# Kernel optimization log

Measured on AMD Instinct MI355X. Metric: run time of the kernel, lower is better.

The kernel has to match this reference:

```python
import jax, jax.numpy as jnp
import numpy as np

N_ITER = 2
EPS = 1e-06
EPS2 = 1e-06
EPS3 = 0.001

B, F, M, T = 8, 513, 8, 512


def setup_inputs() -> dict:
    key = jax.random.key(0)
    k1, k2, k3, k4, k5 = jax.random.split(key, 5)
    r = jax.random.uniform(k1, (B, F, M, T), dtype=jnp.float32) + 0.1  # positive variances
    x_re = jax.random.normal(k2, (B, F, M, T), dtype=jnp.float32)
    x_im = jax.random.normal(k3, (B, F, M, T), dtype=jnp.float32)
    eye = jnp.eye(M, dtype=jnp.float32)
    Q_re = eye + 0.1 * jax.random.normal(k4, (B, F, M, M), dtype=jnp.float32)
    Q_im = 0.1 * jax.random.normal(k5, (B, F, M, M), dtype=jnp.float32)
    return {"r": r, "x_re": x_re, "x_im": x_im, "Q_re": Q_re, "Q_im": Q_im}


def _iss_forward(r, x, Q):
    M_ = x.shape[-2]
    T_ = x.shape[-1]
    # spatial covariance per source k: V[b,f,k,m,n] = sum_t r[b,f,k,t] x[b,f,m,t] conj(x[b,f,n,t]) / T
    V = jnp.einsum('bfkt,bfmt,bfnt->bfkmn', jnp.maximum(r, EPS3).astype(x.dtype), x, jnp.conj(x)) / T_
    trV = jnp.real(jnp.einsum('bfkmm->bfk', V))[..., None, None]  # (B,F,M,1,1)
    V = V + jnp.maximum(trV, 1.0).astype(V.dtype) * EPS * jnp.eye(M_, dtype=V.dtype)
    for _ in range(N_ITER):
        for k in range(M_):
            q = Q[..., k, :]                                       # (B,F,M)
            Vq = jnp.einsum('bfkmn,bfn->bfkm', V, jnp.conj(q))     # (B,F,M,M)
            qVq = jnp.maximum(jnp.real(jnp.einsum('bfm,bfkm->bfk', q, Vq)), EPS2)  # (B,F,M)
            v = jnp.einsum('bfkm,bfkm->bfk', Q, Vq) / qVq.astype(x.dtype)          # (B,F,M)
            v = v.at[..., k].set((1.0 - qVq[..., k] ** (-0.5)).astype(x.dtype))
            Q = Q - v[..., :, None] * q[..., None, :]              # rank-1 update
    Qx = jnp.einsum('bfmn,bfnt->bfmt', Q, x)
    xt = Qx.real ** 2 + Qx.imag ** 2
    scale = jnp.mean(xt, axis=(1, 2, 3), keepdims=True)            # (B,1,1,1)
    xt = xt / scale
    Q = Q / jnp.sqrt(jnp.maximum(scale, 1e-06)).astype(x.dtype)
    return Q, xt


def reference(r, x_re, x_im, Q_re, Q_im):
    x = jax.lax.complex(x_re, x_im)
    Q = jax.lax.complex(Q_re, Q_im)
    return _iss_forward(r, x, Q)
```

## Files before the change

### kernel.cpp

```cpp
#include <hip/hip_runtime.h>
#include <math.h>

#define NBF 4104
#define XT_FLOATS 16809984

__device__ float  d_partials[NBF];
__device__ float  d_scales[8];
__device__ float2 d_Qc[NBF * 64];

#define PA_CROSS(P,N,C) cr[P] += ar*xr4[N].C + ai*xi4[N].C; \
                        ci[P] += ai*xr4[N].C - ar*xi4[N].C;

#define PA_G0(C) { const float rw = fmaxf(rv.C, 1e-3f); float ar, ai;          \
    ar = rw*xr4[0].C; ai = rw*xi4[0].C; d0 += ar*xr4[0].C + ai*xi4[0].C;       \
    PA_CROSS(0,1,C) PA_CROSS(1,2,C) PA_CROSS(2,3,C) PA_CROSS(3,4,C)            \
    PA_CROSS(4,5,C) PA_CROSS(5,6,C) PA_CROSS(6,7,C)                            \
    ar = rw*xr4[7].C; ai = rw*xi4[7].C; d1 += ar*xr4[7].C + ai*xi4[7].C; }

#define PA_G1(C) { const float rw = fmaxf(rv.C, 1e-3f); float ar, ai;          \
    ar = rw*xr4[1].C; ai = rw*xi4[1].C; d0 += ar*xr4[1].C + ai*xi4[1].C;       \
    PA_CROSS(0,2,C) PA_CROSS(1,3,C) PA_CROSS(2,4,C) PA_CROSS(3,5,C)            \
    PA_CROSS(4,6,C) PA_CROSS(5,7,C)                                            \
    ar = rw*xr4[6].C; ai = rw*xi4[6].C; d1 += ar*xr4[6].C + ai*xi4[6].C;       \
    PA_CROSS(6,7,C) }

#define PA_G2(C) { const float rw = fmaxf(rv.C, 1e-3f); float ar, ai;          \
    ar = rw*xr4[2].C; ai = rw*xi4[2].C; d0 += ar*xr4[2].C + ai*xi4[2].C;       \
    PA_CROSS(0,3,C) PA_CROSS(1,4,C) PA_CROSS(2,5,C) PA_CROSS(3,6,C)            \
    PA_CROSS(4,7,C)                                                            \
    ar = rw*xr4[5].C; ai = rw*xi4[5].C; d1 += ar*xr4[5].C + ai*xi4[5].C;       \
    PA_CROSS(5,6,C) PA_CROSS(6,7,C) }

#define PA_G3(C) { const float rw = fmaxf(rv.C, 1e-3f); float ar, ai;          \
    ar = rw*xr4[3].C; ai = rw*xi4[3].C; d0 += ar*xr4[3].C + ai*xi4[3].C;       \
    PA_CROSS(0,4,C) PA_CROSS(1,5,C) PA_CROSS(2,6,C) PA_CROSS(3,7,C)            \
    ar = rw*xr4[4].C; ai = rw*xi4[4].C; d1 += ar*xr4[4].C + ai*xi4[4].C;       \
    PA_CROSS(4,5,C) PA_CROSS(5,6,C) PA_CROSS(6,7,C) }

#define VSTD2(D,M)  s_V[k][M][M] = make_float2((D)*invT, 0.f);
#define VSTO2(P,M,N){ const float vr=cr[P]*invT, vi=ci[P]*invT;  \
                      s_V[k][M][N] = make_float2(vr,  vi);       \
                      s_V[k][N][M] = make_float2(vr, -vi); }

__global__ __launch_bounds__(256, 2) void iss_cov(
    const float* __restrict__ g_r,
    const float* __restrict__ g_xre,
    const float* __restrict__ g_xim,
    const float* __restrict__ g_Qre,
    const float* __restrict__ g_Qim,
    float* __restrict__ g_out,
    const int qmode)
{
    __shared__ float  s_xr[8][512];
    __shared__ float  s_xi[8][512];
    __shared__ float2 s_V[8][8][9];
    __shared__ float2 s_Q[8][8];

    const int tid = threadIdx.x;
    const int bf  = blockIdx.x;
    const size_t base = (size_t)bf * 4096;

    const float* xre = g_xre + base;
    const float* xim = g_xim + base;

    {
        const float4* xr4g = (const float4*)xre;
        const float4* xi4g = (const float4*)xim;
        float4* sxr4 = (float4*)&s_xr[0][0];
        float4* sxi4 = (float4*)&s_xi[0][0];
        #pragma unroll
        for (int i = 0; i < 4; ++i) {
            const int idx = tid + (i << 8);
            sxr4[idx] = xr4g[idx];
            sxi4[idx] = xi4g[idx];
        }
        if (tid < 64)
            s_Q[tid>>3][tid&7] = make_float2(g_Qre[(size_t)bf*64 + tid],
                                             g_Qim[(size_t)bf*64 + tid]);
    }
    __syncthreads();

    const int tl = tid & 7;
    const int k  = (tid >> 3) & 7;
    const int g  = tid >> 6;

    float d0 = 0.f, d1 = 0.f;
    float cr[7], ci[7];
    #pragma unroll
    for (int p = 0; p < 7; ++p) { cr[p] = 0.f; ci[p] = 0.f; }

    {
        const float* rrow = g_r + base + (k << 9);
        #pragma unroll 2
        for (int i = 0; i < 16; ++i) {
            const int t = (i << 5) + (tl << 2);
            const float4 rv = *(const float4*)&rrow[t];
            float4 xr4[8], xi4[8];
            #pragma unroll
            for (int n = 0; n < 8; ++n) {
                xr4[n] = *(const float4*)&s_xr[n][t];
                xi4[n] = *(const float4*)&s_xi[n][t];
            }
            if      (g == 0) { PA_G0(x) PA_G0(y) PA_G0(z) PA_G0(w) }
            else if (g == 1) { PA_G1(x) PA_G1(y) PA_G1(z) PA_G1(w) }
            else if (g == 2) { PA_G2(x) PA_G2(y) PA_G2(z) PA_G2(w) }
            else             { PA_G3(x) PA_G3(y) PA_G3(z) PA_G3(w) }
        }
    }

    #pragma unroll
    for (int off = 1; off < 8; off <<= 1) {
        d0 += __shfl_xor(d0, off, 64);
        d1 += __shfl_xor(d1, off, 64);
        #pragma unroll
        for (int p = 0; p < 7; ++p) {
            cr[p] += __shfl_xor(cr[p], off, 64);
            ci[p] += __shfl_xor(ci[p], off, 64);
        }
    }

    if (tl == 0) {
        const float invT = 1.0f / 512.0f;
        if (g == 0) {
            VSTD2(d0,0) VSTO2(0,0,1) VSTO2(1,0,2) VSTO2(2,0,3) VSTO2(3,0,4)
                        VSTO2(4,0,5) VSTO2(5,0,6) VSTO2(6,0,7)
            VSTD2(d1,7)
        } else if (g == 1) {
            VSTD2(d0,1) VSTO2(0,1,2) VSTO2(1,1,3) VSTO2(2,1,4) VSTO2(3,1,5)
                        VSTO2(4,1,6) VSTO2(5,1,7)
            VSTD2(d1,6) VSTO2(6,6,7)
        } else if (g == 2) {
            VSTD2(d0,2) VSTO2(0,2,3) VSTO2(1,2,4) VSTO2(2,2,5) VSTO2(3,2,6)
                        VSTO2(4,2,7)
            VSTD2(d1,5) VSTO2(5,5,6) VSTO2(6,5,7)
        } else {
            VSTD2(d0,3) VSTO2(0,3,4) VSTO2(1,3,5) VSTO2(2,3,6) VSTO2(3,3,7)
            VSTD2(d1,4) VSTO2(4,4,5) VSTO2(5,4,6) VSTO2(6,4,7)
        }
    }
    __syncthreads();

    if (tid < 64) {
        {
            const int kq = tid >> 3, mq = tid & 7;
            const float dv = s_V[kq][mq][mq].x;
            float tr = dv;
            #pragma unroll
            for (int off = 1; off < 8; off <<= 1) tr += __shfl_xor(tr, off, 64);
            s_V[kq][mq][mq].x = dv + fmaxf(tr, 1.0f) * 1e-6f;
        }
        const int kp = tid >> 3, mm = tid & 7;
        float vRr[8], vRi[8];
        #pragma unroll
        for (int n = 0; n < 8; ++n) {
            const float2 V = s_V[kp][mm][n];
            vRr[n] = V.x; vRi[n] = V.y;
        }
        const float2 Q0 = s_Q[kp][mm];
        float qre = Q0.x, qim = Q0.y;

        #pragma unroll
        for (int step = 0; step < 16; ++step) {
            const int kk = step & 7;
            float qnr[8], qni[8];
            #pragma unroll
            for (int n = 0; n < 8; ++n) {
                qnr[n] = __shfl(qre, (kk<<3)+n, 64);
                qni[n] = __shfl(qim, (kk<<3)+n, 64);
            }
            const float qmr = __shfl(qre, (kk<<3)+mm, 64);
            const float qmi = __shfl(qim, (kk<<3)+mm, 64);

            float vqr = 0.f, vqi = 0.f;
            #pragma unroll
            for (int n = 0; n < 8; ++n) {
                vqr += vRr[n]*qnr[n] + vRi[n]*qni[n];
                vqi += vRi[n]*qnr[n] - vRr[n]*qni[n];
            }
            float p   = qmr*vqr - qmi*vqi;
            float tre = qre*vqr - qim*vqi;
            float tim = qre*vqi + qim*vqr;
            #pragma unroll
            for (int off = 1; off < 8; off <<= 1) {
                p   += __shfl_xor(p,   off, 64);
                tre += __shfl_xor(tre, off, 64);
                tim += __shfl_xor(tim, off, 64);
            }
            const float qvq = fmaxf(p, 1e-6f);
            float vr_, vi_;
            if (kp == kk) { vr_ = 1.0f - rsqrtf(qvq); vi_ = 0.f; }
            else { const float inv = 1.0f / qvq; vr_ = tre*inv; vi_ = tim*inv; }
            qre -= vr_*qmr - vi_*qmi;
            qim -= vr_*qmi + vi_*qmr;
        }

        d_Qc[(size_t)bf*64 + tid] = make_float2(qre, qim);
        if (qmode == 2) {
            g_out[(size_t)bf*128 + tid*2]     = qre;
            g_out[(size_t)bf*128 + tid*2 + 1] = qim;
        } else {
            g_out[(size_t)bf*64 + tid] = qre;
        }
    }
}

__global__ void iss_xt(
    const float* __restrict__ g_xre,
    const float* __restrict__ g_xim,
    float* __restrict__ g_out,
    const int xt_off)
{
    __shared__ float2 s_Q[8][8];
    __shared__ float  sp[2];

    const int tid = threadIdx.x;
    const int bf  = blockIdx.x;
    const size_t base = (size_t)bf * 4096;
    const float* xre = g_xre + base;
    const float* xim = g_xim + base;

    if (tid < 64)
        s_Q[tid>>3][tid&7] = d_Qc[(size_t)bf*64 + tid];
    __syncthreads();

    float* out_xt = g_out + xt_off;
    const int t0 = tid << 2;
    float4 xr4[8], xi4[8];
    #pragma unroll
    for (int n = 0; n < 8; ++n) {
        xr4[n] = *(const float4*)&xre[(n << 9) + t0];
        xi4[n] = *(const float4*)&xim[(n << 9) + t0];
    }
    float lsum = 0.f;
    #pragma unroll
    for (int m = 0; m < 8; ++m) {
        float2 qv[8];
        #pragma unroll
        for (int n = 0; n < 8; ++n) qv[n] = s_Q[m][n];
        float a0=0.f,b0=0.f,a1=0.f,b1=0.f,a2=0.f,b2=0.f,a3=0.f,b3=0.f;
        #pragma unroll
        for (int n = 0; n < 8; ++n) {
            const float qr = qv[n].x, qi = qv[n].y;
            a0 += qr*xr4[n].x - qi*xi4[n].x;  b0 += qr*xi4[n].x + qi*xr4[n].x;
            a1 += qr*xr4[n].y - qi*xi4[n].y;  b1 += qr*xi4[n].y + qi*xr4[n].y;
            a2 += qr*xr4[n].z - qi*xi4[n].z;  b2 += qr*xi4[n].z + qi*xr4[n].z;
            a3 += qr*xr4[n].w - qi*xi4[n].w;  b3 += qr*xi4[n].w + qi*xr4[n].w;
        }
        float4 pw;
        pw.x = a0*a0 + b0*b0;  pw.y = a1*a1 + b1*b1;
        pw.z = a2*a2 + b2*b2;  pw.w = a3*a3 + b3*b3;
        *(float4*)&out_xt[base + (m << 9) + t0] = pw;
        lsum += pw.x + pw.y + pw.z + pw.w;
    }
    #pragma unroll
    for (int off = 32; off >= 1; off >>= 1) lsum += __shfl_xor(lsum, off, 64);
    if ((tid & 63) == 0) sp[tid >> 6] = lsum;
    __syncthreads();
    if (tid == 0) d_partials[bf] = sp[0] + sp[1];
}

__global__ __launch_bounds__(256) void iss_scale()
{
    const int b = blockIdx.x, tid = threadIdx.x;
    __shared__ float sp[4];
    float s = 0.f;
    for (int i = tid; i < 513; i += 256) s += d_partials[b*513 + i];
    #pragma unroll
    for (int off = 32; off >= 1; off >>= 1) s += __shfl_xor(s, off, 64);
    if ((tid & 63) == 0) sp[tid >> 6] = s;
    __syncthreads();
    if (tid == 0) d_scales[b] = (sp[0]+sp[1]+sp[2]+sp[3]) / (513.0f * 8.0f * 512.0f);
}

__global__ __launch_bounds__(256) void iss_norm(
    float* __restrict__ g_out,
    const int nq4,
    const int qb4,
    const int nt4)
{
    float4* o4 = (float4*)g_out;
    for (int i = blockIdx.x*256 + threadIdx.x; i < nt4; i += gridDim.x*256) {
        float s;
        if (i < nq4) {
            const int b = i / qb4;
            s = rsqrtf(fmaxf(d_scales[b], 1e-6f));
        } else {
            const int j = i - nq4;
            const int b = j / 525312;
            s = 1.0f / d_scales[b];
        }
        float4 v = o4[i];
        v.x *= s; v.y *= s; v.z *= s; v.w *= s;
        o4[i] = v;
    }
}

extern "C" void kernel_launch(void* const* d_in, const int* in_sizes, int n_in,
                              void* d_out, int out_size, void* d_ws, size_t ws_size,
                              hipStream_t stream) {
    const float* r   = (const float*)d_in[0];
    const float* xre = (const float*)d_in[1];
    const float* xim = (const float*)d_in[2];
    const float* Qre = (const float*)d_in[3];
    const float* Qim = (const float*)d_in[4];
    float* out = (float*)d_out;

    const int q_floats = out_size - XT_FLOATS;
    const int qmode  = (q_floats >= 525312) ? 2 : 1;
    const int xt_off = (qmode == 2) ? 525312 : 262656;
    const int nq4 = xt_off / 4;
    const int qb4 = xt_off / (4 * 8);
    const int nt4 = nq4 + XT_FLOATS / 4;

    iss_cov  <<<NBF, 256, 0, stream>>>(r, xre, xim, Qre, Qim, out, qmode);
    iss_xt   <<<NBF, 128, 0, stream>>>(xre, xim, out, xt_off);
    iss_scale<<<8,   256, 0, stream>>>();
    iss_norm <<<4096,256, 0, stream>>>(out, nq4, qb4, nt4);
}
```

Baseline: 193.7 us.

## Compute scale partials in cov kernel and fold normalization into xt pass

The power-sum partials are now computed inside the covariance kernel from the x tile already held in shared memory, using the final Q. The scale reduction then runs before the xt kernel, so xt writes normalized outputs and normalized Q directly. This drops the separate in-place normalization pass, which re-read and rewrote roughly 67MB of output. In exchange the Qx product is computed twice, once in cov and again in xt, and cov gains extra work and a barrier.

```diff
diff --git a/kernel.cpp b/kernel.cpp
--- a/kernel.cpp
+++ b/kernel.cpp
@@ -47,14 +47,13 @@
     const float* __restrict__ g_xre,
     const float* __restrict__ g_xim,
     const float* __restrict__ g_Qre,
-    const float* __restrict__ g_Qim,
-    float* __restrict__ g_out,
-    const int qmode)
+    const float* __restrict__ g_Qim)
 {
     __shared__ float  s_xr[8][512];
     __shared__ float  s_xi[8][512];
     __shared__ float2 s_V[8][8][9];
     __shared__ float2 s_Q[8][8];
+    __shared__ float  s_part[4];
 
     const int tid = threadIdx.x;
     const int bf  = blockIdx.x;
@@ -194,24 +193,64 @@
             qim -= vr_*qmi + vi_*qmr;
         }
 
+        s_Q[kp][mm] = make_float2(qre, qim);
         d_Qc[(size_t)bf*64 + tid] = make_float2(qre, qim);
-        if (qmode == 2) {
-            g_out[(size_t)bf*128 + tid*2]     = qre;
-            g_out[(size_t)bf*128 + tid*2 + 1] = qim;
-        } else {
-            g_out[(size_t)bf*64 + tid] = qre;
-        }
-    }
+    }
+    __syncthreads();
+
+    float lsum = 0.f;
+    {
+        const int t0 = tid, t1 = tid + 256;
+        float xra[8], xia[8], xrb[8], xib[8];
+        #pragma unroll
+        for (int n = 0; n < 8; ++n) {
+            xra[n] = s_xr[n][t0];  xia[n] = s_xi[n][t0];
+            xrb[n] = s_xr[n][t1];  xib[n] = s_xi[n][t1];
+        }
+        #pragma unroll
+        for (int m = 0; m < 8; ++m) {
+            float2 qv[8];
+            #pragma unroll
+            for (int n = 0; n < 8; ++n) qv[n] = s_Q[m][n];
+            float ar = 0.f, ai = 0.f, br = 0.f, bi = 0.f;
+            #pragma unroll
+            for (int n = 0; n < 8; ++n) {
+                ar += qv[n].x*xra[n] - qv[n].y*xia[n];
+                ai += qv[n].x*xia[n] + qv[n].y*xra[n];
+                br += qv[n].x*xrb[n] - qv[n].y*xib[n];
+                bi += qv[n].x*xib[n] + qv[n].y*xrb[n];
+            }
+            lsum += ar*ar + ai*ai + br*br + bi*bi;
+        }
+    }
+    #pragma unroll
+    for (int off = 32; off >= 1; off >>= 1) lsum += __shfl_xor(lsum, off, 64);
+    if ((tid & 63) == 0) s_part[tid >> 6] = lsum;
+    __syncthreads();
+    if (tid == 0) d_partials[bf] = s_part[0] + s_part[1] + s_part[2] + s_part[3];
+}
+
+__global__ __launch_bounds__(256) void iss_scale()
+{
+    const int b = blockIdx.x, tid = threadIdx.x;
+    __shared__ float sp[4];
+    float s = 0.f;
+    for (int i = tid; i < 513; i += 256) s += d_partials[b*513 + i];
+    #pragma unroll
+    for (int off = 32; off >= 1; off >>= 1) s += __shfl_xor(s, off, 64);
+    if ((tid & 63) == 0) sp[tid >> 6] = s;
+    __syncthreads();
+    if (tid == 0) d_scales[b] = (sp[0]+sp[1]+sp[2]+sp[3]) / (513.0f * 8.0f * 512.0f);
 }
 
 __global__ void iss_xt(
     const float* __restrict__ g_xre,
     const float* __restrict__ g_xim,
     float* __restrict__ g_out,
+    const int qmode,
     const int xt_off)
 {
     __shared__ float2 s_Q[8][8];
-    __shared__ float  sp[2];
 
     const int tid = threadIdx.x;
     const int bf  = blockIdx.x;
@@ -219,8 +258,20 @@
     const float* xre = g_xre + base;
     const float* xim = g_xim + base;
 
-    if (tid < 64)
-        s_Q[tid>>3][tid&7] = d_Qc[(size_t)bf*64 + tid];
+    const float scale = d_scales[bf / 513];
+    const float invs  = 1.0f / scale;
+
+    if (tid < 64) {
+        const float2 q = d_Qc[(size_t)bf*64 + tid];
+        s_Q[tid>>3][tid&7] = q;
+        const float qn = rsqrtf(fmaxf(scale, 1e-6f));
+        if (qmode == 2) {
+            g_out[(size_t)bf*128 + tid*2]     = q.x * qn;
+            g_out[(size_t)bf*128 + tid*2 + 1] = q.y * qn;
+        } else {
+            g_out[(size_t)bf*64 + tid] = q.x * qn;
+        }
+    }
     __syncthreads();
 
     float* out_xt = g_out + xt_off;
@@ -231,7 +282,6 @@
         xr4[n] = *(const float4*)&xre[(n << 9) + t0];
         xi4[n] = *(const float4*)&xim[(n << 9) + t0];
     }
-    float lsum = 0.f;
     #pragma unroll
     for (int m = 0; m < 8; ++m) {
         float2 qv[8];
@@ -247,51 +297,9 @@
             a3 += qr*xr4[n].w - qi*xi4[n].w;  b3 += qr*xi4[n].w + qi*xr4[n].w;
         }
         float4 pw;
-        pw.x = a0*a0 + b0*b0;  pw.y = a1*a1 + b1*b1;
-        pw.z = a2*a2 + b2*b2;  pw.w = a3*a3 + b3*b3;
+        pw.x = (a0*a0 + b0*b0) * invs;  pw.y = (a1*a1 + b1*b1) * invs;
+        pw.z = (a2*a2 + b2*b2) * invs;  pw.w = (a3*a3 + b3*b3) * invs;
         *(float4*)&out_xt[base + (m << 9) + t0] = pw;
-        lsum += pw.x + pw.y + pw.z + pw.w;
-    }
-    #pragma unroll
-    for (int off = 32; off >= 1; off >>= 1) lsum += __shfl_xor(lsum, off, 64);
-    if ((tid & 63) == 0) sp[tid >> 6] = lsum;
-    __syncthreads();
-    if (tid == 0) d_partials[bf] = sp[0] + sp[1];
-}
-
-__global__ __launch_bounds__(256) void iss_scale()
-{
-    const int b = blockIdx.x, tid = threadIdx.x;
-    __shared__ float sp[4];
-    float s = 0.f;
-    for (int i = tid; i < 513; i += 256) s += d_partials[b*513 + i];
-    #pragma unroll
-    for (int off = 32; off >= 1; off >>= 1) s += __shfl_xor(s, off, 64);
-    if ((tid & 63) == 0) sp[tid >> 6] = s;
-    __syncthreads();
-    if (tid == 0) d_scales[b] = (sp[0]+sp[1]+sp[2]+sp[3]) / (513.0f * 8.0f * 512.0f);
-}
-
-__global__ __launch_bounds__(256) void iss_norm(
-    float* __restrict__ g_out,
-    const int nq4,
-    const int qb4,
-    const int nt4)
-{
-    float4* o4 = (float4*)g_out;
-    for (int i = blockIdx.x*256 + threadIdx.x; i < nt4; i += gridDim.x*256) {
-        float s;
-        if (i < nq4) {
-            const int b = i / qb4;
-            s = rsqrtf(fmaxf(d_scales[b], 1e-6f));
-        } else {
-            const int j = i - nq4;
-            const int b = j / 525312;
-            s = 1.0f / d_scales[b];
-        }
-        float4 v = o4[i];
-        v.x *= s; v.y *= s; v.z *= s; v.w *= s;
-        o4[i] = v;
     }
 }
 
@@ -308,12 +316,8 @@
     const int q_floats = out_size - XT_FLOATS;
     const int qmode  = (q_floats >= 525312) ? 2 : 1;
     const int xt_off = (qmode == 2) ? 525312 : 262656;
-    const int nq4 = xt_off / 4;
-    const int qb4 = xt_off / (4 * 8);
-    const int nt4 = nq4 + XT_FLOATS / 4;
-
-    iss_cov  <<<NBF, 256, 0, stream>>>(r, xre, xim, Qre, Qim, out, qmode);
-    iss_xt   <<<NBF, 128, 0, stream>>>(xre, xim, out, xt_off);
+
+    iss_cov  <<<NBF, 256, 0, stream>>>(r, xre, xim, Qre, Qim);
     iss_scale<<<8,   256, 0, stream>>>();
-    iss_norm <<<4096,256, 0, stream>>>(out, nq4, qb4, nt4);
+    iss_xt   <<<NBF, 128, 0, stream>>>(xre, xim, out, qmode, xt_off);
 }
```

Measured after the change: 199.1 us. 2.8% more time.
